# Kernel tuning notes

Hardware: AMD Instinct MI355X
Metric: run time of the kernel (lower is better)

Reference implementation:

```python
import jax, jax.numpy as jnp
import numpy as np

B, N, C = 4, 4096, 1024
E = 8
K = 2
HIGH = 2            # high_noise_experts
THRESH = 0.5        # snr_threshold
CAP_FACTOR = 1.25
INTER = C * 8 // 3  # 2730


def setup_inputs() -> dict:
    key = jax.random.key(0)
    k = jax.random.split(key, 6)
    return {
        "x": jax.random.normal(k[0], (B, N, C), jnp.float32),
        "cond": jax.random.normal(k[1], (B, C), jnp.float32),
        "snr": jax.random.uniform(k[2], (B,), jnp.float32),
        "gate_w": jax.random.normal(k[3], (2 * C, E), jnp.float32) * 0.02,
        "gate_up_w": jax.random.normal(k[4], (E, C, 2 * INTER), jnp.float32) * 0.02,
        "down_w": jax.random.normal(k[5], (E, INTER, C), jnp.float32) * 0.02,
    }


def _moe_forward(x, cond, snr, gate_w, gate_up_w, down_w):
    b, n, c = x.shape
    x_flat = x.reshape(b * n, c)                       # (T, C)
    cond_flat = jnp.repeat(cond, n, axis=0)            # (T, C)
    snr_flat = jnp.repeat(snr, n)                      # (T,)

    # gating: concat(content, conditioning) -> expert logits
    logits = jnp.concatenate([x_flat, cond_flat], axis=-1) @ gate_w  # (T, E)

    # SNR mask: high-noise tokens may only use experts [0, HIGH)
    high_noise = (snr_flat < THRESH)[:, None]          # (T, 1)
    low_noise_cols = jnp.arange(E) >= HIGH             # (E,)
    logits = logits + jnp.where(high_noise & low_noise_cols, -jnp.inf, 0.0)

    # eval mode: no jitter noise
    probs = jax.nn.softmax(logits, axis=-1)            # (T, E)
    top_probs, top_idx = jax.lax.top_k(probs, K)       # (T, K)
    top_probs = top_probs / jnp.maximum(top_probs.sum(-1, keepdims=True), 1e-12)

    T = b * n
    capacity = max(1, int(CAP_FACTOR * T / E))

    def expert_fn(e, wgu, wd):
        # priority of each (token, slot) for expert e; unassigned -> -inf
        pri = jnp.where(top_idx == e, top_probs, -jnp.inf).reshape(-1)  # (T*K,)
        vals, idx = jax.lax.top_k(pri, capacity)       # capacity-limited select
        tok = idx // K                                 # token index of each slot
        w = jnp.where(jnp.isfinite(vals), vals, 0.0)   # zero weight for padding
        xe = x_flat[tok]                               # (cap, C) gather
        gu = xe @ wgu                                  # (cap, 2*INTER)
        g, u = jnp.split(gu, 2, axis=-1)
        y = (jax.nn.silu(g) * u) @ wd                  # (cap, C)
        return tok, y * w[:, None]

    toks, ys = jax.vmap(expert_fn)(jnp.arange(E), gate_up_w, down_w)
    out = jnp.zeros_like(x_flat).at[toks.reshape(-1)].add(ys.reshape(-1, c))
    return out.reshape(b, n, c)


def reference(x, cond, snr, gate_w, gate_up_w, down_w):
    out = _moe_forward(x, cond, snr, gate_w, gate_up_w, down_w)
    # eval mode: load-balance loss is 0
    return out, jnp.float32(0.0)
```

## Files before the change

kernel.cpp:

```cpp
#include <hip/hip_runtime.h>
#include <hip/hip_bf16.h>
#include <stdint.h>

#define T_TOK 16384
#define CDIM  1024
#define ENUM_ 8
#define INTER_ 2730
#define IPAD  2752
#define NGU   5460
#define NGUPAD 5504
#define CAP   2560
#define EGRP  4
#define CSTRIDE 64

typedef __attribute__((ext_vector_type(8))) short short8;
typedef __attribute__((ext_vector_type(4))) float f32x4;
typedef unsigned long long u64;
typedef unsigned int u32;

static __device__ __forceinline__ ushort f2bf(float f){
  u32 u = __float_as_uint(f);
  u32 r = u + 0x7FFFu + ((u >> 16) & 1u);
  return (ushort)(r >> 16);
}

static __device__ __forceinline__ void glds16(const void* g, void* l){
  __builtin_amdgcn_global_load_lds(
      (const __attribute__((address_space(1))) void*)g,
      (__attribute__((address_space(3))) void*)l, 16, 0, 0);
}

__global__ void k_tr_wgu(const float* __restrict__ wgu, ushort* __restrict__ wguT){
  __shared__ float tile[32][33];
  const int e = blockIdx.z;
  const int k0 = blockIdx.x*32, n0 = blockIdx.y*32;
  const float* src = wgu + (size_t)e*CDIM*NGU;
  ushort* dst = wguT + (size_t)e*NGUPAD*CDIM;
  const int tx = threadIdx.x, ty = threadIdx.y;
  #pragma unroll
  for (int r = ty; r < 32; r += 8){
    int n = n0 + tx;
    int j = (n < IPAD) ? n : n - (IPAD - INTER_);
    bool valid = (n < INTER_) || (n >= IPAD && j < NGU);
    tile[r][tx] = valid ? src[(size_t)(k0 + r)*NGU + j] : 0.f;
  }
  __syncthreads();
  #pragma unroll
  for (int r = ty; r < 32; r += 8)
    dst[(size_t)(n0 + r)*CDIM + k0 + tx] = f2bf(tile[tx][r]);
}

__global__ void k_tr_dwn(const float* __restrict__ dw, ushort* __restrict__ dwT){
  __shared__ float tile[32][33];
  const int e = blockIdx.z;
  const int k0 = blockIdx.x*32, n0 = blockIdx.y*32;
  const float* src = dw + (size_t)e*INTER_*CDIM;
  ushort* dst = dwT + (size_t)e*CDIM*IPAD;
  const int tx = threadIdx.x, ty = threadIdx.y;
  #pragma unroll
  for (int r = ty; r < 32; r += 8){
    int k = k0 + r;
    tile[r][tx] = (k < INTER_) ? src[(size_t)k*CDIM + n0 + tx] : 0.f;
  }
  __syncthreads();
  #pragma unroll
  for (int r = ty; r < 32; r += 8)
    dst[(size_t)(n0 + r)*IPAD + k0 + tx] = f2bf(tile[tx][r]);
}

__global__ void k_cond(const float* __restrict__ cond, const float* __restrict__ gate_w,
                       float* __restrict__ condlog){
  const int b = blockIdx.x;
  const int wave = threadIdx.x >> 6, lane = threadIdx.x & 63;
  float a0 = 0.f, a1 = 0.f;
  for (int c = lane; c < CDIM; c += 64){
    float cv = cond[(size_t)b*CDIM + c];
    const float* g = gate_w + (size_t)(CDIM + c)*8;
    a0 += cv * g[2*wave]; a1 += cv * g[2*wave + 1];
  }
  #pragma unroll
  for (int off = 32; off; off >>= 1){
    a0 += __shfl_down(a0, off, 64);
    a1 += __shfl_down(a1, off, 64);
  }
  if (lane == 0){
    condlog[b*8 + 2*wave]     = a0;
    condlog[b*8 + 2*wave + 1] = a1;
  }
}

__global__ __launch_bounds__(256) void k_gate(
    const float* __restrict__ x, const float* __restrict__ gate_w,
    const float* __restrict__ condlog, const float* __restrict__ snr,
    u32* __restrict__ pcnt, u64* __restrict__ entries, ushort* __restrict__ xb){
  __shared__ float gwT[8*1024];
  __shared__ u32 lcnt[8];
  __shared__ u32 lbase[8];
  __shared__ u64 keybuf[32];
  __shared__ u32 posbuf[32];
  const int tid = threadIdx.x;
  if (tid < 8) lcnt[tid] = 0;
  for (int idx = tid; idx < 8192; idx += 256){
    float v = gate_w[idx];
    gwT[(idx & 7)*1024 + (idx >> 3)] = v;
  }
  __syncthreads();
  const int wave = tid >> 6, lane = tid & 63;
  const int tbase = blockIdx.x*16 + wave*4;
  #pragma unroll 1
  for (int it = 0; it < 4; ++it){
    const int t = tbase + it;
    const int b = t >> 12;
    float acc[8] = {0,0,0,0,0,0,0,0};
    #pragma unroll
    for (int i = 0; i < 4; ++i){
      const int c = lane*4 + 256*i;
      const float4 xv = *(const float4*)(x + (size_t)t*CDIM + c);
      ushort4 xo;
      xo.x = f2bf(xv.x); xo.y = f2bf(xv.y); xo.z = f2bf(xv.z); xo.w = f2bf(xv.w);
      *(ushort4*)(xb + (size_t)t*CDIM + c) = xo;
      #pragma unroll
      for (int e = 0; e < 8; ++e){
        const float4 gv = *(const float4*)(gwT + e*1024 + c);
        acc[e] += xv.x*gv.x + xv.y*gv.y + xv.z*gv.z + xv.w*gv.w;
      }
    }
    #pragma unroll
    for (int e = 0; e < 8; ++e)
      #pragma unroll
      for (int off = 32; off; off >>= 1)
        acc[e] += __shfl_down(acc[e], off, 64);
    if (lane == 0){
      bool hn = snr[b] < 0.5f;
      float lg[8];
      #pragma unroll
      for (int e = 0; e < 8; ++e) lg[e] = acc[e] + condlog[b*8 + e];
      float mx = -1e30f;
      #pragma unroll
      for (int e = 0; e < 8; ++e) if (!(hn && e >= 2) && lg[e] > mx) mx = lg[e];
      float p[8]; float s = 0.f;
      #pragma unroll
      for (int e = 0; e < 8; ++e){ p[e] = (hn && e >= 2) ? 0.f : expf(lg[e] - mx); s += p[e]; }
      float inv_ = 1.f / s;
      #pragma unroll
      for (int e = 0; e < 8; ++e) p[e] *= inv_;
      int i0 = 0;
      #pragma unroll
      for (int e = 1; e < 8; ++e) if (p[e] > p[i0]) i0 = e;
      int i1 = -1; float pv1 = -1.f;
      #pragma unroll
      for (int e = 0; e < 8; ++e) if (e != i0 && p[e] > pv1){ pv1 = p[e]; i1 = e; }
      float v0 = p[i0], v1 = pv1;
      float den = fmaxf(v0 + v1, 1e-12f);
      v0 /= den; v1 /= den;
      u32 flat0 = (u32)(t*2);
      const int slot = wave*4 + it;
      u32 p0 = atomicAdd(&lcnt[i0], 1u);
      u32 p1 = atomicAdd(&lcnt[i1], 1u);
      keybuf[2*slot]     = ((u64)__float_as_uint(v0) << 32) | (u64)(0xFFFFFFFFu - flat0);
      posbuf[2*slot]     = ((u32)i0 << 16) | p0;
      keybuf[2*slot + 1] = ((u64)__float_as_uint(v1) << 32) | (u64)(0xFFFFFFFFu - (flat0 + 1u));
      posbuf[2*slot + 1] = ((u32)i1 << 16) | p1;
    }
  }
  __syncthreads();
  if (tid < 8) lbase[tid] = atomicAdd(&pcnt[tid*CSTRIDE], lcnt[tid]);
  __syncthreads();
  if (tid < 32){
    u32 pe = posbuf[tid];
    int e = (int)(pe >> 16);
    u32 pos = pe & 0xFFFFu;
    entries[(size_t)e*T_TOK + lbase[e] + pos] = keybuf[tid];
  }
}

__global__ void k_select(const u32* __restrict__ pcnt, const u64* __restrict__ entries,
                         u64* __restrict__ thresh){
  const int e = blockIdx.x;
  const int n = (int)pcnt[e*CSTRIDE];
  if (n <= CAP){ if (threadIdx.x == 0) thresh[e] = 0ull; return; }
  const u64* keys = entries + (size_t)e*T_TOK;
  __shared__ u32 hist[256];
  __shared__ u64 spfx;
  __shared__ int srem;
  u64 prefix = 0, pmask = 0;
  int rem = CAP;
  for (int d = 7; d >= 0; --d){
    const int sh = d*8;
    hist[threadIdx.x] = 0;
    __syncthreads();
    for (int i = threadIdx.x; i < n; i += 256){
      u64 k = keys[i];
      if ((k & pmask) == prefix)
        atomicAdd(&hist[(u32)((k >> sh) & 0xFFull)], 1u);
    }
    __syncthreads();
    if (threadIdx.x == 0){
      int c = 0, chosen = 0, nr = rem;
      for (int v = 255; v >= 0; --v){
        int nc = c + (int)hist[v];
        if (nc >= rem){ chosen = v; nr = rem - c; break; }
        c = nc;
      }
      spfx = prefix | ((u64)(u32)chosen << sh);
      srem = nr;
    }
    __syncthreads();
    prefix = spfx; rem = srem; pmask |= (0xFFull << sh);
  }
  if (threadIdx.x == 0) thresh[e] = prefix;
}

__global__ void k_compact(const u32* __restrict__ pcnt, const u64* __restrict__ entries,
                          const u64* __restrict__ thresh, u32* __restrict__ mcnt,
                          int* __restrict__ tokbuf, float* __restrict__ wgtbuf,
                          u32* __restrict__ invcnt, u32* __restrict__ inv){
  const int e = blockIdx.y;
  const int n = (int)pcnt[e*CSTRIDE];
  const u64 th = thresh[e];
  const u64* keys = entries + (size_t)e*T_TOK;
  for (int i = blockIdx.x*256 + threadIdx.x; i < n; i += gridDim.x*256){
    u64 k = keys[i];
    if (k >= th){
      u32 pos = atomicAdd(&mcnt[e], 1u);
      u32 flat = 0xFFFFFFFFu - (u32)(k & 0xFFFFFFFFull);
      int t = (int)(flat >> 1);
      tokbuf[(size_t)e*CAP + pos] = t;
      wgtbuf[(size_t)e*CAP + pos] = __uint_as_float((u32)(k >> 32));
      u32 ic = atomicAdd(&invcnt[t], 1u);
      inv[2*t + ic] = ((u32)e << 12) | pos;
    }
  }
}

__global__ __launch_bounds__(256) void k_gemm1(
    const ushort* __restrict__ xb, const ushort* __restrict__ wguT_g,
    const int* __restrict__ tok_g, const u32* __restrict__ mcnt_g,
    ushort* __restrict__ h_g){
  const int z = blockIdx.z;
  const int m_e = (int)mcnt_g[z];
  const int m0 = blockIdx.x * 128;
  if (m0 >= m_e) return;
  const ushort* wguT = wguT_g + (size_t)z*NGUPAD*CDIM;
  const int* tok = tok_g + (size_t)z*CAP;
  ushort* h = h_g + (size_t)z*CAP*IPAD;
  const int j0 = blockIdx.y * 64;

  __shared__ ushort As[128*32];
  __shared__ ushort Bg[64*32];
  __shared__ ushort Bu[64*32];
  const int tid = threadIdx.x;
  const int lane = tid & 63, wave = tid >> 6;
  const int wm = wave >> 1, wn = wave & 1;
  const int lm = lane & 15, quad = lane >> 4;

  const int af0 = tid*8, af1 = tid*8 + 2048;
  const ushort* ag0 = xb + (size_t)tok[m0 + (af0 >> 5)]*CDIM + (af0 & 31);
  const ushort* ag1 = xb + (size_t)tok[m0 + (af1 >> 5)]*CDIM + (af1 & 31);
  const int br = tid >> 2, bc = (tid & 3)*8;
  const ushort* bgp = wguT + (size_t)(j0 + br)*CDIM + bc;
  const ushort* bup = wguT + (size_t)(IPAD + j0 + br)*CDIM + bc;

  f32x4 accg[4][2], accu[4][2];
  #pragma unroll
  for (int i = 0; i < 4; ++i)
    #pragma unroll
    for (int j = 0; j < 2; ++j){
      accg[i][j] = (f32x4){0.f,0.f,0.f,0.f};
      accu[i][j] = (f32x4){0.f,0.f,0.f,0.f};
    }

  for (int k0 = 0; k0 < CDIM; k0 += 32){
    glds16(ag0 + k0, As + af0);
    glds16(ag1 + k0, As + af1);
    glds16(bgp + k0, Bg + tid*8);
    glds16(bup + k0, Bu + tid*8);
    __syncthreads();
    short8 a[4], vg[2], vu[2];
    #pragma unroll
    for (int mt = 0; mt < 4; ++mt)
      a[mt] = *(const short8*)(As + (wm*64 + mt*16 + lm)*32 + quad*8);
    #pragma unroll
    for (int nt = 0; nt < 2; ++nt){
      vg[nt] = *(const short8*)(Bg + (wn*32 + nt*16 + lm)*32 + quad*8);
      vu[nt] = *(const short8*)(Bu + (wn*32 + nt*16 + lm)*32 + quad*8);
    }
    __syncthreads();
    #pragma unroll
    for (int mt = 0; mt < 4; ++mt)
      #pragma unroll
      for (int nt = 0; nt < 2; ++nt){
        accg[mt][nt] = __builtin_amdgcn_mfma_f32_16x16x32_bf16(a[mt], vg[nt], accg[mt][nt], 0, 0, 0);
        accu[mt][nt] = __builtin_amdgcn_mfma_f32_16x16x32_bf16(a[mt], vu[nt], accu[mt][nt], 0, 0, 0);
      }
  }
  #pragma unroll
  for (int mt = 0; mt < 4; ++mt)
    #pragma unroll
    for (int nt = 0; nt < 2; ++nt)
      #pragma unroll
      for (int r = 0; r < 4; ++r){
        int row = m0 + wm*64 + mt*16 + quad*4 + r;
        int col = j0 + wn*32 + nt*16 + lm;
        float g = accg[mt][nt][r];
        float uu = accu[mt][nt][r];
        float sg = g / (1.f + __expf(-g));
        h[(size_t)row*IPAD + col] = f2bf(sg * uu);
      }
}

__global__ __launch_bounds__(256) void k_gemm2(
    const ushort* __restrict__ h_g, const ushort* __restrict__ dwT_g,
    const u32* __restrict__ mcnt_g, float* __restrict__ y_g){
  const int z = blockIdx.z;
  const int m_e = (int)mcnt_g[z];
  const int m0 = blockIdx.x * 128;
  if (m0 >= m_e) return;
  const ushort* h = h_g + (size_t)z*CAP*IPAD;
  const ushort* dwT = dwT_g + (size_t)z*CDIM*IPAD;
  const int n0 = blockIdx.y * 64;

  __shared__ ushort As[128*32];
  __shared__ ushort Bs[64*32];
  const int tid = threadIdx.x;
  const int lane = tid & 63, wave = tid >> 6;
  const int wm = wave >> 1, wn = wave & 1;
  const int lm = lane & 15, quad = lane >> 4;

  const int af0 = tid*8, af1 = tid*8 + 2048;
  const ushort* ap0 = h + (size_t)(m0 + (af0 >> 5))*IPAD + (af0 & 31);
  const ushort* ap1 = h + (size_t)(m0 + (af1 >> 5))*IPAD + (af1 & 31);
  const int br = tid >> 2, bc = (tid & 3)*8;
  const ushort* bp = dwT + (size_t)(n0 + br)*IPAD + bc;

  f32x4 acc[4][2];
  #pragma unroll
  for (int i = 0; i < 4; ++i)
    #pragma unroll
    for (int j = 0; j < 2; ++j) acc[i][j] = (f32x4){0.f,0.f,0.f,0.f};

  for (int k0 = 0; k0 < IPAD; k0 += 32){
    glds16(ap0 + k0, As + af0);
    glds16(ap1 + k0, As + af1);
    glds16(bp + k0, Bs + tid*8);
    __syncthreads();
    short8 a[4], b[2];
    #pragma unroll
    for (int mt = 0; mt < 4; ++mt)
      a[mt] = *(const short8*)(As + (wm*64 + mt*16 + lm)*32 + quad*8);
    #pragma unroll
    for (int nt = 0; nt < 2; ++nt)
      b[nt] = *(const short8*)(Bs + (wn*32 + nt*16 + lm)*32 + quad*8);
    __syncthreads();
    #pragma unroll
    for (int mt = 0; mt < 4; ++mt)
      #pragma unroll
      for (int nt = 0; nt < 2; ++nt)
        acc[mt][nt] = __builtin_amdgcn_mfma_f32_16x16x32_bf16(a[mt], b[nt], acc[mt][nt], 0, 0, 0);
  }
  #pragma unroll
  for (int mt = 0; mt < 4; ++mt)
    #pragma unroll
    for (int r = 0; r < 4; ++r){
      int row = m0 + wm*64 + mt*16 + quad*4 + r;
      float* yrow = y_g + ((size_t)z*CAP + row)*CDIM;
      #pragma unroll
      for (int nt = 0; nt < 2; ++nt){
        int col = n0 + wn*32 + nt*16 + lm;
        yrow[col] = acc[mt][nt][r];
      }
    }
}

__global__ __launch_bounds__(256) void k_out(
    const float* __restrict__ ybuf, const u32* __restrict__ inv,
    const u32* __restrict__ invcnt, const float* __restrict__ wgtbuf,
    float* __restrict__ out){
  const int t = blockIdx.x*4 + (threadIdx.x >> 6);
  const int lane = threadIdx.x & 63;
  const int n = (int)invcnt[t];
  f32x4 acc[4];
  #pragma unroll
  for (int i = 0; i < 4; ++i) acc[i] = (f32x4){0.f,0.f,0.f,0.f};
  for (int j = 0; j < n; ++j){
    u32 v = inv[2*t + j];
    int e = (int)(v >> 12);
    int pos = (int)(v & 0xFFFu);
    float w = wgtbuf[e*CAP + pos];
    const float* yr = ybuf + ((size_t)e*CAP + pos)*CDIM;
    #pragma unroll
    for (int i = 0; i < 4; ++i){
      f32x4 yv = *(const f32x4*)(yr + i*256 + lane*4);
      acc[i] += yv * w;
    }
  }
  float* orow = out + (size_t)t*CDIM;
  #pragma unroll
  for (int i = 0; i < 4; ++i)
    *(f32x4*)(orow + i*256 + lane*4) = acc[i];
}

extern "C" void kernel_launch(void* const* d_in, const int* in_sizes, int n_in,
                              void* d_out, int out_size, void* d_ws, size_t ws_size,
                              hipStream_t stream){
  const float* x      = (const float*)d_in[0];
  const float* cond   = (const float*)d_in[1];
  const float* snr    = (const float*)d_in[2];
  const float* gate_w = (const float*)d_in[3];
  const float* wgu    = (const float*)d_in[4];
  const float* wdn    = (const float*)d_in[5];
  float* out = (float*)d_out;
  (void)in_sizes; (void)n_in; (void)ws_size; (void)out_size;

  char* ws = (char*)d_ws;
  size_t off = 0;
  auto take = [&](size_t bytes) -> char* {
    char* p = ws + off;
    off += (bytes + 255) & ~(size_t)255;
    return p;
  };
  u32* pcnt     = (u32*)take(8*CSTRIDE*4);
  u32* mcnt     = (u32*)take(256);
  float* condlog = (float*)take(256);
  u64* thresh   = (u64*)take(256);
  u32* invcnt   = (u32*)take((size_t)T_TOK*4);
  u32* inv      = (u32*)take((size_t)T_TOK*2*4);
  u64* entries  = (u64*)take((size_t)ENUM_*T_TOK*8);
  int* tokbuf   = (int*)take((size_t)ENUM_*CAP*4);
  float* wgtbuf = (float*)take((size_t)ENUM_*CAP*4);
  ushort* xb    = (ushort*)take((size_t)T_TOK*CDIM*2);
  ushort* wguT  = (ushort*)take((size_t)ENUM_*NGUPAD*CDIM*2);
  ushort* dwT   = (ushort*)take((size_t)ENUM_*CDIM*IPAD*2);
  ushort* hbuf  = (ushort*)take((size_t)EGRP*CAP*IPAD*2);
  float* ybuf   = (float*)take((size_t)ENUM_*CAP*CDIM*4);

  hipMemsetAsync(pcnt, 0, 68352, stream);
  hipMemsetAsync(tokbuf, 0, (size_t)ENUM_*CAP*4, stream);

  k_cond<<<4, 256, 0, stream>>>(cond, gate_w, condlog);
  k_gate<<<T_TOK/16, 256, 0, stream>>>(x, gate_w, condlog, snr, pcnt, entries, xb);
  k_tr_wgu<<<dim3(CDIM/32, NGUPAD/32, ENUM_), dim3(32,8), 0, stream>>>(wgu, wguT);
  k_tr_dwn<<<dim3(IPAD/32, CDIM/32, ENUM_), dim3(32,8), 0, stream>>>(wdn, dwT);
  k_select<<<ENUM_, 256, 0, stream>>>(pcnt, entries, thresh);
  k_compact<<<dim3(64, ENUM_), 256, 0, stream>>>(pcnt, entries, thresh, mcnt,
                                                 tokbuf, wgtbuf, invcnt, inv);

  for (int g = 0; g < ENUM_/EGRP; ++g){
    k_gemm1<<<dim3(CAP/128, IPAD/64, EGRP), 256, 0, stream>>>(
        xb, wguT + (size_t)g*EGRP*NGUPAD*CDIM,
        tokbuf + (size_t)g*EGRP*CAP, mcnt + g*EGRP, hbuf);
    k_gemm2<<<dim3(CAP/128, CDIM/64, EGRP), 256, 0, stream>>>(
        hbuf, dwT + (size_t)g*EGRP*CDIM*IPAD,
        mcnt + g*EGRP, ybuf + (size_t)g*EGRP*CAP*CDIM);
  }
  k_out<<<T_TOK/4, 256, 0, stream>>>(ybuf, inv, invcnt, wgtbuf, out);
}
```

Before: 1.055 ms.

## Rewrite gate-up GEMM with 256x128 tiles, double-buffered swizzled LDS pipeline

The gate/up expert GEMM kernel moves from 128x64 tiles with a single-stage LDS load to 256x128 tiles at 512 threads. It uses a two-stage double-buffered 128KB LDS ring with XOR-swizzled layout, interleaving global-to-LDS prefetch with MFMA phases under explicit barriers, waitcnt and setprio. The intent is to raise arithmetic intensity, hide global load latency and avoid LDS bank conflicts. The intermediate padding grows (IPAD 2816, NGUPAD 5632) so the larger tiles divide evenly, which adds some wasted compute and memory, and the large LDS footprint limits occupancy.

```diff
diff --git a/kernel.cpp b/kernel.cpp
--- a/kernel.cpp
+++ b/kernel.cpp
@@ -6,9 +6,9 @@
 #define CDIM  1024
 #define ENUM_ 8
 #define INTER_ 2730
-#define IPAD  2752
+#define IPAD  2816
 #define NGU   5460
-#define NGUPAD 5504
+#define NGUPAD 5632
 #define CAP   2560
 #define EGRP  4
 #define CSTRIDE 64
@@ -233,80 +233,131 @@
   }
 }
 
-__global__ __launch_bounds__(256) void k_gemm1(
+static __device__ __forceinline__ void mf16(f32x4 (&acc)[4][4],
+                                            const short8 (&a)[4], const short8 (&b)[4]){
+  #pragma unroll
+  for (int mt = 0; mt < 4; ++mt)
+    #pragma unroll
+    for (int ct = 0; ct < 4; ++ct)
+      acc[mt][ct] = __builtin_amdgcn_mfma_f32_16x16x32_bf16(a[mt], b[ct], acc[mt][ct], 0, 0, 0);
+}
+
+#define BAR do{ asm volatile("" ::: "memory"); __builtin_amdgcn_s_barrier(); \
+                asm volatile("" ::: "memory"); }while(0)
+#define VW2 asm volatile("s_waitcnt vmcnt(2)" ::: "memory")
+
+__global__ __launch_bounds__(512, 2) void k_gemm1(
     const ushort* __restrict__ xb, const ushort* __restrict__ wguT_g,
     const int* __restrict__ tok_g, const u32* __restrict__ mcnt_g,
     ushort* __restrict__ h_g){
   const int z = blockIdx.z;
   const int m_e = (int)mcnt_g[z];
-  const int m0 = blockIdx.x * 128;
+  const int m0 = blockIdx.x * 256;
   if (m0 >= m_e) return;
   const ushort* wguT = wguT_g + (size_t)z*NGUPAD*CDIM;
   const int* tok = tok_g + (size_t)z*CAP;
   ushort* h = h_g + (size_t)z*CAP*IPAD;
-  const int j0 = blockIdx.y * 64;
-
-  __shared__ ushort As[128*32];
-  __shared__ ushort Bg[64*32];
-  __shared__ ushort Bu[64*32];
+  const int j0 = blockIdx.y * 128;
+
+  __shared__ __attribute__((aligned(128))) char lds[131072];
   const int tid = threadIdx.x;
   const int lane = tid & 63, wave = tid >> 6;
-  const int wm = wave >> 1, wn = wave & 1;
+  const int wm = wave >> 1, wc = wave & 1;
   const int lm = lane & 15, quad = lane >> 4;
 
-  const int af0 = tid*8, af1 = tid*8 + 2048;
-  const ushort* ag0 = xb + (size_t)tok[m0 + (af0 >> 5)]*CDIM + (af0 & 31);
-  const ushort* ag1 = xb + (size_t)tok[m0 + (af1 >> 5)]*CDIM + (af1 & 31);
-  const int br = tid >> 2, bc = (tid & 3)*8;
-  const ushort* bgp = wguT + (size_t)(j0 + br)*CDIM + bc;
-  const ushort* bup = wguT + (size_t)(IPAD + j0 + br)*CDIM + bc;
-
-  f32x4 accg[4][2], accu[4][2];
+  const int d0 = tid*16, d1 = tid*16 + 8192;
+  const int lb0 = d0 ^ (((d0 >> 7) & 7) << 4);
+  const int lb1 = d1 ^ (((d1 >> 7) & 7) << 4);
+  const int r0 = lb0 >> 7, c0 = (lb0 & 127) >> 1;
+  const int r1 = lb1 >> 7, c1 = (lb1 & 127) >> 1;
+  const ushort* ap00 = xb + (size_t)tok[m0 + r0]*CDIM + c0;
+  const ushort* ap01 = xb + (size_t)tok[m0 + r1]*CDIM + c1;
+  const ushort* ap10 = xb + (size_t)tok[m0 + 128 + r0]*CDIM + c0;
+  const ushort* ap11 = xb + (size_t)tok[m0 + 128 + r1]*CDIM + c1;
+  const ushort* bp00 = wguT + (size_t)(j0 + r0)*CDIM + c0;
+  const ushort* bp01 = wguT + (size_t)(j0 + r1)*CDIM + c1;
+  const ushort* bp10 = wguT + (size_t)(IPAD + j0 + r0)*CDIM + c0;
+  const ushort* bp11 = wguT + (size_t)(IPAD + j0 + r1)*CDIM + c1;
+
+#define STAGE_A(s, hf, ke) do{ \
+    glds16(((hf) ? ap10 : ap00) + (ke), lds + (s)*32768 + (hf)*16384 + d0); \
+    glds16(((hf) ? ap11 : ap01) + (ke), lds + (s)*32768 + (hf)*16384 + d1); }while(0)
+#define STAGE_B(s, pl, ke) do{ \
+    glds16(((pl) ? bp10 : bp00) + (ke), lds + 65536 + (s)*32768 + (pl)*16384 + d0); \
+    glds16(((pl) ? bp11 : bp01) + (ke), lds + 65536 + (s)*32768 + (pl)*16384 + d1); }while(0)
+
+  int aoff[4][2], boff[4][2];
+  #pragma unroll
+  for (int mt = 0; mt < 4; ++mt)
+    #pragma unroll
+    for (int ks = 0; ks < 2; ++ks){
+      int lba = ((wm & 1)*64 + mt*16 + lm)*128 + ks*64 + quad*16;
+      aoff[mt][ks] = (wm >> 1)*16384 + (lba ^ (((lba >> 7) & 7) << 4));
+      int lbb = (wc*64 + mt*16 + lm)*128 + ks*64 + quad*16;
+      boff[mt][ks] = lbb ^ (((lbb >> 7) & 7) << 4);
+    }
+
+#define RD(off) (*(const short8*)(lds + (off)))
+#define LOAD_A(s, ks) do{ a[0]=RD((s)*32768+aoff[0][ks]); a[1]=RD((s)*32768+aoff[1][ks]); \
+                          a[2]=RD((s)*32768+aoff[2][ks]); a[3]=RD((s)*32768+aoff[3][ks]); }while(0)
+#define LOAD_B(s, pl, ks) do{ \
+    b[0]=RD(65536+(s)*32768+(pl)*16384+boff[0][ks]); b[1]=RD(65536+(s)*32768+(pl)*16384+boff[1][ks]); \
+    b[2]=RD(65536+(s)*32768+(pl)*16384+boff[2][ks]); b[3]=RD(65536+(s)*32768+(pl)*16384+boff[3][ks]); }while(0)
+
+  f32x4 accg[4][4], accu[4][4];
   #pragma unroll
   for (int i = 0; i < 4; ++i)
     #pragma unroll
-    for (int j = 0; j < 2; ++j){
+    for (int j = 0; j < 4; ++j){
       accg[i][j] = (f32x4){0.f,0.f,0.f,0.f};
       accu[i][j] = (f32x4){0.f,0.f,0.f,0.f};
     }
-
-  for (int k0 = 0; k0 < CDIM; k0 += 32){
-    glds16(ag0 + k0, As + af0);
-    glds16(ag1 + k0, As + af1);
-    glds16(bgp + k0, Bg + tid*8);
-    glds16(bup + k0, Bu + tid*8);
-    __syncthreads();
-    short8 a[4], vg[2], vu[2];
-    #pragma unroll
-    for (int mt = 0; mt < 4; ++mt)
-      a[mt] = *(const short8*)(As + (wm*64 + mt*16 + lm)*32 + quad*8);
-    #pragma unroll
-    for (int nt = 0; nt < 2; ++nt){
-      vg[nt] = *(const short8*)(Bg + (wn*32 + nt*16 + lm)*32 + quad*8);
-      vu[nt] = *(const short8*)(Bu + (wn*32 + nt*16 + lm)*32 + quad*8);
-    }
-    __syncthreads();
-    #pragma unroll
-    for (int mt = 0; mt < 4; ++mt)
-      #pragma unroll
-      for (int nt = 0; nt < 2; ++nt){
-        accg[mt][nt] = __builtin_amdgcn_mfma_f32_16x16x32_bf16(a[mt], vg[nt], accg[mt][nt], 0, 0, 0);
-        accu[mt][nt] = __builtin_amdgcn_mfma_f32_16x16x32_bf16(a[mt], vu[nt], accu[mt][nt], 0, 0, 0);
-      }
-  }
+  short8 a[4], b[4];
+
+  STAGE_A(0,0,0); STAGE_A(0,1,0); STAGE_B(0,0,0); STAGE_B(0,1,0);
+  VW2;
+  BAR;
+
+  #pragma unroll 1
+  for (int i = 0; i < CDIM/128; ++i){
+    const int ke1 = (2*i + 1)*64;
+    const int ke2 = ((2*i + 2) & (CDIM/64 - 1))*64;
+    STAGE_A(1,0,ke1); LOAD_A(0,0); LOAD_B(0,0,0);
+    BAR; __builtin_amdgcn_s_setprio(1); mf16(accg, a, b); __builtin_amdgcn_s_setprio(0); VW2; BAR;
+    STAGE_A(1,1,ke1); LOAD_B(0,1,0);
+    BAR; __builtin_amdgcn_s_setprio(1); mf16(accu, a, b); __builtin_amdgcn_s_setprio(0); BAR;
+    STAGE_B(1,0,ke1); LOAD_A(0,1); LOAD_B(0,0,1);
+    BAR; __builtin_amdgcn_s_setprio(1); mf16(accg, a, b); __builtin_amdgcn_s_setprio(0); BAR;
+    STAGE_B(1,1,ke1); LOAD_B(0,1,1);
+    BAR; __builtin_amdgcn_s_setprio(1); mf16(accu, a, b); __builtin_amdgcn_s_setprio(0); VW2; BAR;
+    STAGE_A(0,0,ke2); LOAD_A(1,0); LOAD_B(1,0,0);
+    BAR; __builtin_amdgcn_s_setprio(1); mf16(accg, a, b); __builtin_amdgcn_s_setprio(0); VW2; BAR;
+    STAGE_A(0,1,ke2); LOAD_B(1,1,0);
+    BAR; __builtin_amdgcn_s_setprio(1); mf16(accu, a, b); __builtin_amdgcn_s_setprio(0); BAR;
+    STAGE_B(0,0,ke2); LOAD_A(1,1); LOAD_B(1,0,1);
+    BAR; __builtin_amdgcn_s_setprio(1); mf16(accg, a, b); __builtin_amdgcn_s_setprio(0); BAR;
+    STAGE_B(0,1,ke2); LOAD_B(1,1,1);
+    BAR; __builtin_amdgcn_s_setprio(1); mf16(accu, a, b); __builtin_amdgcn_s_setprio(0); VW2; BAR;
+  }
+
   #pragma unroll
   for (int mt = 0; mt < 4; ++mt)
     #pragma unroll
-    for (int nt = 0; nt < 2; ++nt)
+    for (int ct = 0; ct < 4; ++ct)
       #pragma unroll
       for (int r = 0; r < 4; ++r){
         int row = m0 + wm*64 + mt*16 + quad*4 + r;
-        int col = j0 + wn*32 + nt*16 + lm;
-        float g = accg[mt][nt][r];
-        float uu = accu[mt][nt][r];
+        int col = j0 + wc*64 + ct*16 + lm;
+        float g = accg[mt][ct][r];
+        float uu = accu[mt][ct][r];
         float sg = g / (1.f + __expf(-g));
         h[(size_t)row*IPAD + col] = f2bf(sg * uu);
       }
+#undef STAGE_A
+#undef STAGE_B
+#undef RD
+#undef LOAD_A
+#undef LOAD_B
 }
 
 __global__ __launch_bounds__(256) void k_gemm2(
@@ -446,7 +497,7 @@
                                                  tokbuf, wgtbuf, invcnt, inv);
 
   for (int g = 0; g < ENUM_/EGRP; ++g){
-    k_gemm1<<<dim3(CAP/128, IPAD/64, EGRP), 256, 0, stream>>>(
+    k_gemm1<<<dim3(CAP/256, IPAD/128, EGRP), 512, 0, stream>>>(
         xb, wguT + (size_t)g*EGRP*NGUPAD*CDIM,
         tokbuf + (size_t)g*EGRP*CAP, mcnt + g*EGRP, hbuf);
     k_gemm2<<<dim3(CAP/128, CDIM/64, EGRP), 256, 0, stream>>>(
```

After: 1.002 ms. 1.05x faster.
